# Kernel tuning notes

Measured on AMD Instinct MI355X. Metric: run time of the kernel, lower is better.

## Reference

```python
import jax, jax.numpy as jnp
import numpy as np

NUM_CLASSES = 21
EPS = 1e-6
MOMENTUM = 0.99
K_WEAK = 16
K_STRONG = 256
PROB_THRESH = 0.95
IGNORE = 255
NEG = -1e30


def _normalize(x, axis=-1):
    # matches F.normalize(p=2) / CosineSimilarity with eps=1e-6
    n = jnp.linalg.norm(x, axis=axis, keepdims=True)
    return x / jnp.maximum(n, EPS)


def setup_inputs() -> dict:
    key = jax.random.key(0)
    k0, k1, k2, k3, k4, k5 = jax.random.split(key, 6)
    B, C, H, W = 8, 256, 128, 128
    feature_weak = jax.random.normal(k0, (B, C, H, W), jnp.float32)
    feature_strong = jax.random.normal(k1, (B, C, H, W), jnp.float32)
    probablity_weak = jax.random.uniform(k2, (B, H, W), jnp.float32)
    memory_bank = jax.random.normal(k3, (NUM_CLASSES, 1, C), jnp.float32)
    pred_weak = jax.random.randint(k4, (B, H, W), 0, NUM_CLASSES)
    ignore_mask = jax.random.randint(k5, (B, H, W), 0, 256)
    return {
        'feature_weak': feature_weak,
        'feature_strong': feature_strong,
        'probablity_weak': probablity_weak,
        'memory_bank': memory_bank,
        'pred_weak': pred_weak,
        'ignore_mask': ignore_mask,
    }


def reference(feature_weak, feature_strong, probablity_weak, memory_bank, pred_weak, ignore_mask):
    B, C, H, W = feature_weak.shape
    N = B * H * W
    fw = feature_weak.transpose(0, 2, 3, 1).reshape(N, C)   # weak pixel feats
    fs = feature_strong.transpose(0, 2, 3, 1).reshape(N, C) # strong pixel feats
    seg = pred_weak.reshape(N)
    ign = ignore_mask.reshape(N)  # same-size bilinear resize (align_corners) is identity
    prob = probablity_weak.reshape(N)

    valid = ign != IGNORE
    conf = valid & (prob > PROB_THRESH)

    cls = jnp.arange(NUM_CLASSES)
    is_cls = seg[None, :] == cls[:, None]        # [K, N]
    m_weak = is_cls & conf[None, :]              # per-class high-confidence mask
    m_strong = is_cls & valid[None, :]
    n_weak = m_weak.sum(axis=1)                  # [K]
    n_strong = m_strong.sum(axis=1)

    protos = memory_bank[:, 0, :]                # [K, C]
    pn = _normalize(protos)
    sim_w = _normalize(fw) @ pn.T                # [N, K] cos(pixel_weak, proto)
    sim_s = _normalize(fs) @ pn.T                # [N, K] cos(pixel_strong, proto)

    sw = jnp.where(m_weak, sim_w.T, NEG)         # [K, N]
    ss = jnp.where(m_strong, -sim_s.T, NEG)      # negate -> bottom-k via top_k
    _, idx_w = jax.lax.top_k(sw, K_WEAK)         # [K, 16] most-similar weak pixels
    _, idx_s = jax.lax.top_k(ss, K_STRONG)       # [K, 256] least-similar strong pixels

    # select_feature duplicates the top element: slots are ranks [0,0,1,...,14]
    ranks = jnp.maximum(jnp.arange(K_WEAK) - 1, 0)
    sel_w = fw[idx_w[:, ranks]]                  # [K, 16, C]
    sel_s = fs[idx_s]                            # [K, 256, C]

    kw = jnp.minimum(K_WEAK, n_weak)
    ks = jnp.minimum(K_STRONG, n_strong)
    valid_w = jnp.arange(K_WEAK)[None, :] < kw[:, None]     # [K, 16]
    valid_s = jnp.arange(K_STRONG)[None, :] < ks[:, None]   # [K, 256]

    # calculate_loss: weak side detached, max over strong dim, sum / strong count
    wn = _normalize(jax.lax.stop_gradient(sel_w))
    sn = _normalize(sel_s)
    cosm = jnp.einsum('kwc,ksc->kws', wn, sn)    # [K, 16, 256]
    cosm = jnp.where(valid_s[:, None, :], cosm, NEG)
    max_sim = jnp.where(valid_w, cosm.max(axis=2), 0.0)     # [K, 16]
    class_ok = (n_weak > 0) & (n_strong > 0)
    sim_sum = jnp.where(class_ok, max_sim.sum(axis=1), 0.0).sum()
    count = jnp.where(class_ok, ks, 0).sum()
    loss = jnp.where(count > 0, 1.0 - sim_sum / count, 0.0)

    # update_memory: per-class mean of high-confidence weak feats, EMA scatter
    fw_ng = jax.lax.stop_gradient(fw)            # .data copy -> no grad
    wsum = m_weak.astype(fw.dtype) @ fw_ng       # [K, C] segmented sum
    mean = wsum / jnp.maximum(n_weak, 1).astype(fw.dtype)[:, None]
    new_protos = jnp.where((n_weak > 0)[:, None],
                           MOMENTUM * protos + (1.0 - MOMENTUM) * mean,
                           protos)
    new_memory_bank = new_protos[:, None, :]     # [K, 1, C]
    return loss, new_memory_bank
```

## Files before the change

kernel.cpp:

```cpp
#include <hip/hip_runtime.h>
#include <stdint.h>

#define NCLS  21
#define CDIM  256
#define HWSZ  16384
#define NPIX  131072
#define EPSV  1e-6f
#define NEGV  -1e30f
#define CAP_W 4096
#define CAP_S 16384
#define KSEL  256
#define NCC   8
#define CCH   (CDIM/NCC)
#define NPART 8
#define NBLK2 (NPIX/512)
#define P2    2048
#define NPG   (NPIX/P2)

__device__ __forceinline__ uint64_t pack_key(float v, unsigned idx) {
  unsigned u = __float_as_uint(v);
  u = (u & 0x80000000u) ? ~u : (u | 0x80000000u);
  return ((uint64_t)(~u) << 32) | (uint64_t)idx;
}

__global__ void k0_init(const float* __restrict__ mb, float* pn, float* wsum,
                        int* wcnt, int* scnt) {
  int k = blockIdx.x, t = threadIdx.x;
  float v = mb[k * CDIM + t];
  float s = v * v;
  for (int o = 32; o > 0; o >>= 1) s += __shfl_down(s, o, 64);
  __shared__ float wsh[4];
  int wid = t >> 6, lane = t & 63;
  if (lane == 0) wsh[wid] = s;
  __syncthreads();
  float tot = wsh[0] + wsh[1] + wsh[2] + wsh[3];
  float inv = 1.0f / fmaxf(sqrtf(tot), EPSV);
  pn[k * CDIM + t] = v * inv;
  wsum[k * CDIM + t] = 0.0f;
  if (k == 0 && t < 2 * NCLS) {
    if (t < NCLS) wcnt[t] = 0; else scnt[t - NCLS] = 0;
  }
}

__global__ __launch_bounds__(256, 2)
void k1a_stream(const float* __restrict__ fw, const float* __restrict__ fs,
                const float* __restrict__ prob, const int* __restrict__ seg,
                const int* __restrict__ ign, const float* __restrict__ pn,
                float* part, float* wsum) {
  __shared__ float pnT[CCH * NCLS];
  __shared__ float wloc[NCLS * (CCH + 1)];
  int t = threadIdx.x;
  int pg = blockIdx.x;
  int cc = blockIdx.y;
  int c0 = cc * CCH;
  for (int i = t; i < CCH * NCLS; i += 256) {
    int c = i / NCLS, k = i % NCLS;
    pnT[i] = pn[k * CDIM + c0 + c];
  }
  for (int i = t; i < NCLS * (CCH + 1); i += 256) wloc[i] = 0.0f;
  __syncthreads();

  int base = pg * P2;
  int b = base >> 14;
  int hwb = (base & (HWSZ - 1)) + t;

  int sgv[8]; bool cf[8];
  float dw[8], nw[8], dsv[8], nsv[8];
#pragma unroll
  for (int i = 0; i < 8; ++i) {
    int px = base + i * 256 + t;
    sgv[i] = seg[px];
    int igv = ign[px];
    float prv = prob[px];
    cf[i] = (igv != 255) && (prv > 0.95f);
    dw[i] = nw[i] = dsv[i] = nsv[i] = 0.0f;
  }

  const float* fwp = fw + ((size_t)b * CDIM + c0) * HWSZ + hwb;
  const float* fsp = fs + ((size_t)b * CDIM + c0) * HWSZ + hwb;

#pragma unroll 4
  for (int c = 0; c < CCH; ++c) {
    size_t co = (size_t)c * HWSZ;
    float a[8], s8[8];
#pragma unroll
    for (int i = 0; i < 8; ++i) a[i] = fwp[co + i * 256];
#pragma unroll
    for (int i = 0; i < 8; ++i) s8[i] = fsp[co + i * 256];
#pragma unroll
    for (int i = 0; i < 8; ++i) {
      float p = pnT[c * NCLS + sgv[i]];
      dw[i]  = fmaf(a[i],  p,     dw[i]);
      nw[i]  = fmaf(a[i],  a[i],  nw[i]);
      dsv[i] = fmaf(s8[i], p,     dsv[i]);
      nsv[i] = fmaf(s8[i], s8[i], nsv[i]);
      if (cf[i]) atomicAdd(&wloc[sgv[i] * (CCH + 1) + c], a[i]);
    }
  }

  float4* pp = (float4*)part + (size_t)cc * NPIX + base + t;
#pragma unroll
  for (int i = 0; i < 8; ++i)
    pp[i * 256] = make_float4(dw[i], nw[i], dsv[i], nsv[i]);

  __syncthreads();
  for (int i = t; i < NCLS * CCH; i += 256) {
    int k = i / CCH, cl = i % CCH;
    float v = wloc[k * (CCH + 1) + cl];
    if (v != 0.0f) atomicAdd(&wsum[k * CDIM + c0 + cl], v);
  }
}

__global__ void k1b_write(const float* __restrict__ part, const float* __restrict__ prob,
                          const int* __restrict__ seg, const int* __restrict__ ign,
                          int* wcnt, int* scnt, uint64_t* wkeys, uint64_t* skeys) {
  __shared__ int cs[NCLS], cw[NCLS], bs[NCLS], bw[NCLS];
  int t = threadIdx.x, pg = blockIdx.x;
  for (int i = t; i < NCLS; i += 256) { cs[i] = 0; cw[i] = 0; }
  __syncthreads();
  int n0 = pg * 512 + t * 2;
  int2   sg = *(const int2*)(seg + n0);
  int2   ig = *(const int2*)(ign + n0);
  float2 pr = *(const float2*)(prob + n0);
  float dw[2] = {0,0}, nw[2] = {0,0}, ds[2] = {0,0}, ns[2] = {0,0};
#pragma unroll
  for (int cc = 0; cc < NCC; ++cc) {
    const float4* pp = (const float4*)part + ((size_t)cc * NPIX + n0);
#pragma unroll
    for (int i = 0; i < 2; ++i) {
      float4 v = pp[i];
      dw[i] += v.x; nw[i] += v.y; ds[i] += v.z; ns[i] += v.w;
    }
  }
  int   sga[2] = {sg.x, sg.y};
  int   iga[2] = {ig.x, ig.y};
  float pra[2] = {pr.x, pr.y};
  bool  va[2], cfv[2];
  int   lsl[2] = {0,0}, lwl[2] = {0,0};
#pragma unroll
  for (int i = 0; i < 2; ++i) {
    va[i]  = (iga[i] != 255);
    cfv[i] = va[i] && (pra[i] > 0.95f);
    if (va[i])  lsl[i] = atomicAdd(&cs[sga[i]], 1);
    if (cfv[i]) lwl[i] = atomicAdd(&cw[sga[i]], 1);
  }
  __syncthreads();
  if (t < NCLS) {
    bs[t] = atomicAdd(&scnt[t], cs[t]);
    bw[t] = atomicAdd(&wcnt[t], cw[t]);
  }
  __syncthreads();
#pragma unroll
  for (int i = 0; i < 2; ++i) {
    if (va[i]) {
      int q = sga[i];
      float sim_s = ds[i] / fmaxf(sqrtf(ns[i]), EPSV);
      int pos = bs[q] + lsl[i];
      if (pos < CAP_S) skeys[(size_t)q * CAP_S + pos] = pack_key(-sim_s, (unsigned)(n0 + i));
      if (cfv[i]) {
        float sim_w = dw[i] / fmaxf(sqrtf(nw[i]), EPSV);
        int pw = bw[q] + lwl[i];
        if (pw < CAP_W) wkeys[(size_t)q * CAP_W + pw] = pack_key(sim_w, (unsigned)(n0 + i));
      }
    }
  }
}

__device__ void select_topk(const uint64_t* __restrict__ list, int cnt,
                            uint64_t* T, uint64_t* P, int* pcnt, int* woff) {
  int t = threadIdx.x;
  T[t] = ~0ull;
  if (t == 0) *pcnt = 0;
  __syncthreads();
  for (int base = 0; base < cnt; base += 256) {
    uint64_t key = (base + t < cnt) ? list[base + t] : ~0ull;
    uint64_t cutoff = T[KSEL - 1];
    bool pred = key < cutoff;
    unsigned long long mask = __ballot(pred);
    int wid = t >> 6, lane = t & 63;
    if (lane == 0) woff[wid] = __popcll(mask);
    int prefix = __popcll(mask & ((1ull << lane) - 1ull));
    __syncthreads();
    int off = 0;
    for (int w2 = 0; w2 < wid; ++w2) off += woff[w2];
    int total = woff[0] + woff[1] + woff[2] + woff[3];
    int old = *pcnt;
    if (pred) P[old + off + prefix] = key;
    int newc = old + total;
    __syncthreads();
    if (t == 0) *pcnt = newc;
    bool last = (base + 256 >= cnt);
    if (newc >= KSEL || (last && newc > 0)) {
      for (int i2 = t; i2 < 2 * KSEL; i2 += 256)
        if (i2 >= newc) P[i2] = ~0ull;
      for (unsigned size = 2; size <= 2 * KSEL; size <<= 1) {
        for (unsigned stride = size >> 1; stride > 0; stride >>= 1) {
          __syncthreads();
          unsigned lo = stride - 1;
          unsigned i = (((unsigned)t & ~lo) << 1) | ((unsigned)t & lo);
          unsigned j = i | stride;
          uint64_t a = P[i], b = P[j];
          bool up = ((i & size) == 0);
          if ((a > b) == up) { P[i] = b; P[j] = a; }
        }
      }
      __syncthreads();
      uint64_t a = T[t], b = P[KSEL - 1 - t];
      T[t] = a < b ? a : b;
      for (unsigned stride = KSEL / 2; stride > 0; stride >>= 1) {
        __syncthreads();
        if (((unsigned)t & stride) == 0) {
          uint64_t x = T[t], y = T[t + stride];
          if (x > y) { T[t] = y; T[t + stride] = x; }
        }
      }
      __syncthreads();
      if (t == 0) *pcnt = 0;
      __syncthreads();
    } else {
      __syncthreads();
    }
  }
}

__global__ void k2_topk(const uint64_t* __restrict__ wkeys, const uint64_t* __restrict__ skeys,
                        const int* wcnt, const int* scnt,
                        uint64_t* psel, int* idxw) {
  __shared__ uint64_t T[KSEL];
  __shared__ uint64_t P[2 * KSEL];
  __shared__ int pcnt;
  __shared__ int woff[4];
  int bid = blockIdx.x, t = threadIdx.x;
  if (bid < NCLS * NPART) {
    int k = bid / NPART, p = bid % NPART;
    int cnt = min(scnt[k], CAP_S);
    int chunk = (cnt + NPART - 1) / NPART;
    int lo = p * chunk;
    int hi = min(lo + chunk, cnt);
    int c = hi > lo ? hi - lo : 0;
    select_topk(skeys + (size_t)k * CAP_S + lo, c, T, P, &pcnt, woff);
    psel[((size_t)k * NPART + p) * KSEL + t] = T[t];
  } else {
    int k = bid - NCLS * NPART;
    int cnt = min(wcnt[k], CAP_W);
    select_topk(wkeys + (size_t)k * CAP_W, cnt, T, P, &pcnt, woff);
    if (t < 16) idxw[k * 16 + t] = (int)(unsigned)(T[t] & 0xFFFFFFFFull);
  }
}

__global__ void k2m_merge(const uint64_t* __restrict__ psel, int* idxs) {
  int k = blockIdx.x, t = threadIdx.x;
  __shared__ uint64_t M[NPART * KSEL];
  __shared__ uint64_t M2[4 * KSEL];
  for (int i = t; i < NPART * KSEL; i += 256) M[i] = psel[(size_t)k * NPART * KSEL + i];
  __syncthreads();
#pragma unroll
  for (int p = 0; p < 4; ++p) {
    uint64_t a = M[p * 512 + t], b = M[p * 512 + 511 - t];
    M2[p * 256 + t] = a < b ? a : b;
  }
  for (int str = 128; str > 0; str >>= 1) {
    __syncthreads();
    for (int q = t; q < 4 * 128; q += 256) {
      int list = q >> 7, r = q & 127;
      int i = ((r & ~(str - 1)) << 1) | (r & (str - 1));
      int ai = list * 256 + i, bi = ai + str;
      uint64_t x = M2[ai], y = M2[bi];
      if (x > y) { M2[ai] = y; M2[bi] = x; }
    }
  }
  __syncthreads();
#pragma unroll
  for (int p = 0; p < 2; ++p) {
    uint64_t a = M2[p * 512 + t], b = M2[p * 512 + 511 - t];
    M[p * 256 + t] = a < b ? a : b;
  }
  for (int str = 128; str > 0; str >>= 1) {
    __syncthreads();
    {
      int q = t;
      int list = q >> 7, r = q & 127;
      int i = ((r & ~(str - 1)) << 1) | (r & (str - 1));
      int ai = list * 256 + i, bi = ai + str;
      uint64_t x = M[ai], y = M[bi];
      if (x > y) { M[ai] = y; M[bi] = x; }
    }
  }
  __syncthreads();
  {
    uint64_t a = M[t], b = M[511 - t];
    M2[t] = a < b ? a : b;
  }
  for (int str = 128; str > 0; str >>= 1) {
    __syncthreads();
    if (t < 128) {
      int r = t;
      int i = ((r & ~(str - 1)) << 1) | (r & (str - 1));
      uint64_t x = M2[i], y = M2[i + str];
      if (x > y) { M2[i] = y; M2[i + str] = x; }
    }
  }
  __syncthreads();
  idxs[k * KSEL + t] = (int)(unsigned)(M2[t] & 0xFFFFFFFFull);
}

__global__ void k3a_gather(const float* __restrict__ fw, const float* __restrict__ fs,
                           const int* __restrict__ idxw, const int* __restrict__ idxs,
                           const int* __restrict__ wcnt, const int* __restrict__ scnt,
                           float* dw_dense, float* ds_dense) {
  int k = blockIdx.y;
  int s0 = blockIdx.x * 4;
  int t = threadIdx.x;
  int wid = t >> 6, lane = t & 63;
  int kw_ = min(wcnt[k], 16);
  int ks_ = min(scnt[k], KSEL);
  float v[4];
  bool strong[4];
  int slot_[4];
#pragma unroll
  for (int j = 0; j < 4; ++j) {
    int slot = s0 + j;
    slot_[j] = slot;
    strong[j] = slot < KSEL;
    bool ok;
    int n = 0;
    if (strong[j]) {
      ok = slot < ks_;
      if (ok) n = idxs[k * KSEL + slot];
    } else {
      int i = slot - KSEL;
      ok = i < kw_;
      int rank = i > 0 ? i - 1 : 0;
      if (ok) n = idxw[k * 16 + rank];
    }
    v[j] = 0.0f;
    if (ok) {
      int b = n >> 14, hw = n & (HWSZ - 1);
      const float* f = strong[j] ? fs : fw;
      v[j] = f[(size_t)(b * CDIM + t) * HWSZ + hw];
    }
  }
  __shared__ float wsh[4][4];
  float s[4];
#pragma unroll
  for (int j = 0; j < 4; ++j) {
    s[j] = v[j] * v[j];
    for (int o = 32; o > 0; o >>= 1) s[j] += __shfl_down(s[j], o, 64);
  }
  if (lane == 0) {
#pragma unroll
    for (int j = 0; j < 4; ++j) wsh[wid][j] = s[j];
  }
  __syncthreads();
#pragma unroll
  for (int j = 0; j < 4; ++j) {
    float tot = wsh[0][j] + wsh[1][j] + wsh[2][j] + wsh[3][j];
    float inv = 1.0f / fmaxf(sqrtf(tot), EPSV);
    float out = v[j] * inv;
    if (strong[j]) ds_dense[((size_t)k * KSEL + slot_[j]) * CDIM + t] = out;
    else           dw_dense[((size_t)k * 16 + (slot_[j] - KSEL)) * CDIM + t] = out;
  }
}

__global__ void k3b_loss(const float* __restrict__ dw_dense, const float* __restrict__ ds_dense,
                         const int* __restrict__ scnt, float* pmax) {
  int p = blockIdx.x, k = blockIdx.y, t = threadIdx.x;
  __shared__ float wn[16 * CDIM];
  for (int i = t; i < 16 * CDIM; i += 64) wn[i] = dw_dense[(size_t)k * 16 * CDIM + i];
  __syncthreads();
  int ks_ = min(scnt[k], KSEL);
  int slot = p * 64 + t;
  bool jv = slot < ks_;
  float dots[16];
#pragma unroll
  for (int i = 0; i < 16; ++i) dots[i] = 0.0f;
  if (jv) {
    const float4* sp = (const float4*)(ds_dense + ((size_t)k * KSEL + slot) * CDIM);
    for (int c4 = 0; c4 < CDIM / 4; ++c4) {
      float4 v = sp[c4];
#pragma unroll
      for (int i = 0; i < 16; ++i) {
        float4 w = ((const float4*)(wn + i * CDIM))[c4];
        dots[i] = fmaf(v.x, w.x, dots[i]);
        dots[i] = fmaf(v.y, w.y, dots[i]);
        dots[i] = fmaf(v.z, w.z, dots[i]);
        dots[i] = fmaf(v.w, w.w, dots[i]);
      }
    }
  }
#pragma unroll
  for (int i = 0; i < 16; ++i) {
    float v = jv ? dots[i] : NEGV;
    for (int o = 32; o > 0; o >>= 1) v = fmaxf(v, __shfl_down(v, o, 64));
    if (t == 0) pmax[((size_t)k * 4 + p) * 16 + i] = v;
  }
}

__global__ void k4_final(const float* __restrict__ mb, const float* __restrict__ wsum,
                         const int* __restrict__ wcnt, const int* __restrict__ scnt,
                         const float* __restrict__ pmax, float* out) {
  int k = blockIdx.x, t = threadIdx.x;
  float p = mb[k * CDIM + t];
  float o = p;
  int nw = wcnt[k];
  if (nw > 0) {
    float mean = wsum[k * CDIM + t] / (float)nw;
    o = 0.99f * p + 0.01f * mean;
  }
  out[1 + k * CDIM + t] = o;
  if (k == 0) {
    __shared__ float stot;
    __shared__ int ctot;
    if (t == 0) { stot = 0.0f; ctot = 0; }
    __syncthreads();
    float part = 0.0f;
    int cpart = 0;
    for (int idx = t; idx < NCLS * 16; idx += 256) {
      int q = idx >> 4, i = idx & 15;
      int nwq = wcnt[q], nsq = scnt[q];
      if (nwq > 0 && nsq > 0 && i < min(nwq, 16)) {
        float m =    pmax[((size_t)q * 4 + 0) * 16 + i];
        m = fmaxf(m, pmax[((size_t)q * 4 + 1) * 16 + i]);
        m = fmaxf(m, pmax[((size_t)q * 4 + 2) * 16 + i]);
        m = fmaxf(m, pmax[((size_t)q * 4 + 3) * 16 + i]);
        part += m;
      }
    }
    if (t < NCLS) {
      if (wcnt[t] > 0 && scnt[t] > 0) cpart = min(scnt[t], KSEL);
    }
    for (int o2 = 32; o2 > 0; o2 >>= 1) {
      part += __shfl_down(part, o2, 64);
      cpart += __shfl_down(cpart, o2, 64);
    }
    if ((t & 63) == 0) { atomicAdd(&stot, part); atomicAdd(&ctot, cpart); }
    __syncthreads();
    if (t == 0) out[0] = (ctot > 0) ? (1.0f - stot / (float)ctot) : 0.0f;
  }
}

extern "C" void kernel_launch(void* const* d_in, const int* in_sizes, int n_in,
                              void* d_out, int out_size, void* d_ws, size_t ws_size,
                              hipStream_t stream) {
  const float* fw   = (const float*)d_in[0];
  const float* fs   = (const float*)d_in[1];
  const float* prob = (const float*)d_in[2];
  const float* mb   = (const float*)d_in[3];
  const int*   seg  = (const int*)d_in[4];
  const int*   ign  = (const int*)d_in[5];
  float* out = (float*)d_out;

  char* ws = (char*)d_ws;
  size_t off = 0;
  auto alloc = [&](size_t bytes) -> char* {
    char* p = ws + off;
    off = (off + bytes + 255) & ~(size_t)255;
    return p;
  };
  float*    pn       = (float*)alloc(NCLS * CDIM * 4);
  float*    wsum     = (float*)alloc(NCLS * CDIM * 4);
  int*      wcnt     = (int*)alloc(NCLS * 4);
  int*      scnt     = (int*)alloc(NCLS * 4);
  int*      idxw     = (int*)alloc(NCLS * 16 * 4);
  int*      idxs     = (int*)alloc(NCLS * KSEL * 4);
  float*    pmax     = (float*)alloc(NCLS * 4 * 16 * 4);
  uint64_t* wkeys    = (uint64_t*)alloc((size_t)NCLS * CAP_W * 8);
  uint64_t* skeys    = (uint64_t*)alloc((size_t)NCLS * CAP_S * 8);
  uint64_t* psel     = (uint64_t*)alloc((size_t)NCLS * NPART * KSEL * 8);
  float*    dw_dense = (float*)alloc((size_t)NCLS * 16 * CDIM * 4);
  float*    ds_dense = (float*)alloc((size_t)NCLS * KSEL * CDIM * 4);
  float*    part     = (float*)alloc((size_t)NCC * NPIX * 4 * 4);
  (void)in_sizes; (void)n_in; (void)out_size; (void)ws_size;

  k0_init<<<NCLS, 256, 0, stream>>>(mb, pn, wsum, wcnt, scnt);
  k1a_stream<<<dim3(NPG, NCC), 256, 0, stream>>>(fw, fs, prob, seg, ign, pn,
                                                 part, wsum);
  k1b_write<<<NBLK2, 256, 0, stream>>>(part, prob, seg, ign, wcnt, scnt,
                                       wkeys, skeys);
  k2_topk<<<NCLS * NPART + NCLS, 256, 0, stream>>>(wkeys, skeys, wcnt, scnt,
                                                   psel, idxw);
  k2m_merge<<<NCLS, 256, 0, stream>>>(psel, idxs);
  k3a_gather<<<dim3((KSEL + 16) / 4, NCLS), 256, 0, stream>>>(fw, fs, idxw, idxs,
                                                              wcnt, scnt,
                                                              dw_dense, ds_dense);
  k3b_loss<<<dim3(4, NCLS), 64, 0, stream>>>(dw_dense, ds_dense, scnt, pmax);
  k4_final<<<NCLS, 256, 0, stream>>>(mb, wsum, wcnt, scnt, pmax, out);
}
```

Baseline: 392.5 us.

## Fuse gather into merge and loss kernels using precomputed pixel inverse norms

Stores per-pixel inverse L2 norms for weak and strong features while the partial sums are reduced in k1b. The weak top-16 gather moves into the merge kernel, and the loss kernel now reads strong features straight from the input and scales its dot products by the stored norm. This removes the separate gather kernel, its dense strong buffer round trip and one launch. The loss kernel now uses 256 threads with the channel dimension split across waves plus a shared-memory reduction, in exchange for strided scattered global reads inside it.

```diff
diff --git a/kernel.cpp b/kernel.cpp
--- a/kernel.cpp
+++ b/kernel.cpp
@@ -113,7 +113,8 @@
 
 __global__ void k1b_write(const float* __restrict__ part, const float* __restrict__ prob,
                           const int* __restrict__ seg, const int* __restrict__ ign,
-                          int* wcnt, int* scnt, uint64_t* wkeys, uint64_t* skeys) {
+                          int* wcnt, int* scnt, uint64_t* wkeys, uint64_t* skeys,
+                          float* rnorm_w, float* rnorm_s) {
   __shared__ int cs[NCLS], cw[NCLS], bs[NCLS], bw[NCLS];
   int t = threadIdx.x, pg = blockIdx.x;
   for (int i = t; i < NCLS; i += 256) { cs[i] = 0; cw[i] = 0; }
@@ -132,6 +133,11 @@
       dw[i] += v.x; nw[i] += v.y; ds[i] += v.z; ns[i] += v.w;
     }
   }
+  float2 rw = { 1.0f / fmaxf(sqrtf(nw[0]), EPSV), 1.0f / fmaxf(sqrtf(nw[1]), EPSV) };
+  float2 rs = { 1.0f / fmaxf(sqrtf(ns[0]), EPSV), 1.0f / fmaxf(sqrtf(ns[1]), EPSV) };
+  *(float2*)(rnorm_w + n0) = rw;
+  *(float2*)(rnorm_s + n0) = rs;
+
   int   sga[2] = {sg.x, sg.y};
   int   iga[2] = {ig.x, ig.y};
   float pra[2] = {pr.x, pr.y};
@@ -248,8 +254,24 @@
   }
 }
 
-__global__ void k2m_merge(const uint64_t* __restrict__ psel, int* idxs) {
+__global__ void k2m_merge(const uint64_t* __restrict__ psel, const int* __restrict__ wcnt,
+                          const int* __restrict__ idxw, const float* __restrict__ fw,
+                          const float* __restrict__ rnorm_w,
+                          int* idxs, float* dw_dense) {
   int k = blockIdx.x, t = threadIdx.x;
+  int kw_ = min(wcnt[k], 16);
+  float wv[16];
+#pragma unroll
+  for (int i = 0; i < 16; ++i) {
+    wv[i] = 0.0f;
+    if (i < kw_) {
+      int ri = i > 0 ? i - 1 : 0;
+      int n = idxw[k * 16 + ri];
+      int b = n >> 14, hw = n & (HWSZ - 1);
+      float v = fw[((size_t)b * CDIM + t) * HWSZ + hw];
+      wv[i] = v * rnorm_w[n];
+    }
+  }
   __shared__ uint64_t M[NPART * KSEL];
   __shared__ uint64_t M2[4 * KSEL];
   for (int i = t; i < NPART * KSEL; i += 256) M[i] = psel[(size_t)k * NPART * KSEL + i];
@@ -302,97 +324,72 @@
   }
   __syncthreads();
   idxs[k * KSEL + t] = (int)(unsigned)(M2[t] & 0xFFFFFFFFull);
-}
-
-__global__ void k3a_gather(const float* __restrict__ fw, const float* __restrict__ fs,
-                           const int* __restrict__ idxw, const int* __restrict__ idxs,
-                           const int* __restrict__ wcnt, const int* __restrict__ scnt,
-                           float* dw_dense, float* ds_dense) {
-  int k = blockIdx.y;
-  int s0 = blockIdx.x * 4;
-  int t = threadIdx.x;
-  int wid = t >> 6, lane = t & 63;
-  int kw_ = min(wcnt[k], 16);
-  int ks_ = min(scnt[k], KSEL);
-  float v[4];
-  bool strong[4];
-  int slot_[4];
-#pragma unroll
-  for (int j = 0; j < 4; ++j) {
-    int slot = s0 + j;
-    slot_[j] = slot;
-    strong[j] = slot < KSEL;
-    bool ok;
-    int n = 0;
-    if (strong[j]) {
-      ok = slot < ks_;
-      if (ok) n = idxs[k * KSEL + slot];
-    } else {
-      int i = slot - KSEL;
-      ok = i < kw_;
-      int rank = i > 0 ? i - 1 : 0;
-      if (ok) n = idxw[k * 16 + rank];
-    }
-    v[j] = 0.0f;
-    if (ok) {
-      int b = n >> 14, hw = n & (HWSZ - 1);
-      const float* f = strong[j] ? fs : fw;
-      v[j] = f[(size_t)(b * CDIM + t) * HWSZ + hw];
-    }
-  }
-  __shared__ float wsh[4][4];
-  float s[4];
-#pragma unroll
-  for (int j = 0; j < 4; ++j) {
-    s[j] = v[j] * v[j];
-    for (int o = 32; o > 0; o >>= 1) s[j] += __shfl_down(s[j], o, 64);
-  }
-  if (lane == 0) {
-#pragma unroll
-    for (int j = 0; j < 4; ++j) wsh[wid][j] = s[j];
-  }
-  __syncthreads();
-#pragma unroll
-  for (int j = 0; j < 4; ++j) {
-    float tot = wsh[0][j] + wsh[1][j] + wsh[2][j] + wsh[3][j];
-    float inv = 1.0f / fmaxf(sqrtf(tot), EPSV);
-    float out = v[j] * inv;
-    if (strong[j]) ds_dense[((size_t)k * KSEL + slot_[j]) * CDIM + t] = out;
-    else           dw_dense[((size_t)k * 16 + (slot_[j] - KSEL)) * CDIM + t] = out;
-  }
-}
-
-__global__ void k3b_loss(const float* __restrict__ dw_dense, const float* __restrict__ ds_dense,
+#pragma unroll
+  for (int i = 0; i < 16; ++i)
+    dw_dense[((size_t)k * 16 + i) * CDIM + t] = wv[i];
+}
+
+__global__ void k3f_loss(const float* __restrict__ fs, const float* __restrict__ dw_dense,
+                         const int* __restrict__ idxs, const float* __restrict__ rnorm_s,
                          const int* __restrict__ scnt, float* pmax) {
   int p = blockIdx.x, k = blockIdx.y, t = threadIdx.x;
-  __shared__ float wn[16 * CDIM];
-  for (int i = t; i < 16 * CDIM; i += 64) wn[i] = dw_dense[(size_t)k * 16 * CDIM + i];
-  __syncthreads();
+  __shared__ float wnS[16 * CDIM];
+  __shared__ float pd[4][64][16];
+  for (int i = t; i < 16 * CDIM; i += 256) wnS[i] = dw_dense[(size_t)k * 16 * CDIM + i];
+
   int ks_ = min(scnt[k], KSEL);
-  int slot = p * 64 + t;
+  int j = t & 63, cseg = t >> 6;
+  int slot = p * 64 + j;
   bool jv = slot < ks_;
-  float dots[16];
-#pragma unroll
-  for (int i = 0; i < 16; ++i) dots[i] = 0.0f;
+  int n = 0;
+  float rn = 0.0f;
   if (jv) {
-    const float4* sp = (const float4*)(ds_dense + ((size_t)k * KSEL + slot) * CDIM);
-    for (int c4 = 0; c4 < CDIM / 4; ++c4) {
-      float4 v = sp[c4];
+    n = idxs[k * KSEL + slot];
+    rn = rnorm_s[n];
+  }
+  int b = n >> 14, hw = n & (HWSZ - 1);
+  const float* sp = fs + ((size_t)b * CDIM + cseg * 64) * HWSZ + hw;
+
+  float acc[16];
+#pragma unroll
+  for (int i = 0; i < 16; ++i) acc[i] = 0.0f;
+  __syncthreads();
+
+  if (jv) {
+#pragma unroll 4
+    for (int c4 = 0; c4 < 16; ++c4) {
+      float v0 = sp[(size_t)(4 * c4 + 0) * HWSZ];
+      float v1 = sp[(size_t)(4 * c4 + 1) * HWSZ];
+      float v2 = sp[(size_t)(4 * c4 + 2) * HWSZ];
+      float v3 = sp[(size_t)(4 * c4 + 3) * HWSZ];
 #pragma unroll
       for (int i = 0; i < 16; ++i) {
-        float4 w = ((const float4*)(wn + i * CDIM))[c4];
-        dots[i] = fmaf(v.x, w.x, dots[i]);
-        dots[i] = fmaf(v.y, w.y, dots[i]);
-        dots[i] = fmaf(v.z, w.z, dots[i]);
-        dots[i] = fmaf(v.w, w.w, dots[i]);
+        float4 w = ((const float4*)(wnS + i * CDIM + cseg * 64))[c4];
+        acc[i] = fmaf(v0, w.x, acc[i]);
+        acc[i] = fmaf(v1, w.y, acc[i]);
+        acc[i] = fmaf(v2, w.z, acc[i]);
+        acc[i] = fmaf(v3, w.w, acc[i]);
       }
     }
   }
 #pragma unroll
-  for (int i = 0; i < 16; ++i) {
-    float v = jv ? dots[i] : NEGV;
-    for (int o = 32; o > 0; o >>= 1) v = fmaxf(v, __shfl_down(v, o, 64));
-    if (t == 0) pmax[((size_t)k * 4 + p) * 16 + i] = v;
+  for (int i = 0; i < 16; ++i) pd[cseg][j][i] = acc[i];
+  __syncthreads();
+
+  int lane = t & 63, w = t >> 6;
+  float mv[4];
+#pragma unroll
+  for (int q = 0; q < 4; ++q) {
+    int i = w * 4 + q;
+    float d = pd[0][lane][i] + pd[1][lane][i] + pd[2][lane][i] + pd[3][lane][i];
+    d *= rn;
+    mv[q] = jv ? d : NEGV;
+    for (int o = 32; o > 0; o >>= 1) mv[q] = fmaxf(mv[q], __shfl_down(mv[q], o, 64));
+  }
+  if (lane == 0) {
+#pragma unroll
+    for (int q = 0; q < 4; ++q)
+      pmax[((size_t)k * 4 + p) * 16 + w * 4 + q] = mv[q];
   }
 }
 
@@ -464,11 +461,12 @@
   int*      idxw     = (int*)alloc(NCLS * 16 * 4);
   int*      idxs     = (int*)alloc(NCLS * KSEL * 4);
   float*    pmax     = (float*)alloc(NCLS * 4 * 16 * 4);
+  float*    rnorm_w  = (float*)alloc((size_t)NPIX * 4);
+  float*    rnorm_s  = (float*)alloc((size_t)NPIX * 4);
   uint64_t* wkeys    = (uint64_t*)alloc((size_t)NCLS * CAP_W * 8);
   uint64_t* skeys    = (uint64_t*)alloc((size_t)NCLS * CAP_S * 8);
   uint64_t* psel     = (uint64_t*)alloc((size_t)NCLS * NPART * KSEL * 8);
   float*    dw_dense = (float*)alloc((size_t)NCLS * 16 * CDIM * 4);
-  float*    ds_dense = (float*)alloc((size_t)NCLS * KSEL * CDIM * 4);
   float*    part     = (float*)alloc((size_t)NCC * NPIX * 4 * 4);
   (void)in_sizes; (void)n_in; (void)out_size; (void)ws_size;
 
@@ -476,13 +474,12 @@
   k1a_stream<<<dim3(NPG, NCC), 256, 0, stream>>>(fw, fs, prob, seg, ign, pn,
                                                  part, wsum);
   k1b_write<<<NBLK2, 256, 0, stream>>>(part, prob, seg, ign, wcnt, scnt,
-                                       wkeys, skeys);
+                                       wkeys, skeys, rnorm_w, rnorm_s);
   k2_topk<<<NCLS * NPART + NCLS, 256, 0, stream>>>(wkeys, skeys, wcnt, scnt,
                                                    psel, idxw);
-  k2m_merge<<<NCLS, 256, 0, stream>>>(psel, idxs);
-  k3a_gather<<<dim3((KSEL + 16) / 4, NCLS), 256, 0, stream>>>(fw, fs, idxw, idxs,
-                                                              wcnt, scnt,
-                                                              dw_dense, ds_dense);
-  k3b_loss<<<dim3(4, NCLS), 64, 0, stream>>>(dw_dense, ds_dense, scnt, pmax);
+  k2m_merge<<<NCLS, 256, 0, stream>>>(psel, wcnt, idxw, fw, rnorm_w,
+                                      idxs, dw_dense);
+  k3f_loss<<<dim3(4, NCLS), 256, 0, stream>>>(fs, dw_dense, idxs, rnorm_s,
+                                              scnt, pmax);
   k4_final<<<NCLS, 256, 0, stream>>>(mb, wsum, wcnt, scnt, pmax, out);
 }
```

Result: faster. 382.5 us (-2.6%).
